# Kernel tuning notes

Measured on AMD Instinct MI355X. Metric: run time of the kernel, lower is better.

The kernel has to match this reference:

```python
import jax, jax.numpy as jnp
import numpy as np

N = 50000      # nodes
E = 800000     # edges (avg degree 16)
D = 128        # in_channels == hidden_channels (required by x*M + x_hat*~M)
OUT = 64       # fc out_channels


def _linear_params(key, out_f, in_f):
    # torch.nn.Linear default init: U(-1/sqrt(in), 1/sqrt(in))
    bound = 1.0 / np.sqrt(in_f)
    kw, kb = jax.random.split(key)
    W = jax.random.uniform(kw, (out_f, in_f), jnp.float32, -bound, bound)
    b = jax.random.uniform(kb, (out_f,), jnp.float32, -bound, bound)
    return W, b


def setup_inputs() -> dict:
    key = jax.random.key(0)
    ks = jax.random.split(key, 8)
    x = jax.random.normal(ks[0], (N, D), jnp.float32)
    edge_index = jax.random.randint(ks[1], (2, E), 0, N, dtype=jnp.int64)
    edge_weight = jax.random.uniform(ks[2], (E,), jnp.float32)
    M = jax.random.randint(ks[3], (N, D), 0, 2) > 0  # bool mask
    W1, b1 = _linear_params(ks[4], D, D)
    W2, b2 = _linear_params(ks[5], D, D)
    W3, b3 = _linear_params(ks[6], D, D)
    Wf, bf = _linear_params(ks[7], OUT, D)
    # extra Parameter `bias` in each FPLayer is zero-initialized
    z = jnp.zeros((D,), jnp.float32)
    return {"edge_index": edge_index, "edge_weight": edge_weight, "x": x, "M": M,
            "W1": W1, "b1": b1, "bias1": z, "W2": W2, "b2": b2, "bias2": z,
            "W3": W3, "b3": b3, "bias3": z, "Wf": Wf, "bf": bf}


def reference(edge_index, edge_weight, x, M,
              W1, b1, bias1, W2, b2, bias2, W3, b3, bias3, Wf, bf):
    row, col = edge_index[0], edge_index[1]
    n = x.shape[0]
    # symmetric degree normalization based on destination-node in-degree
    deg = jax.ops.segment_sum(jnp.ones(row.shape[0], x.dtype), col, num_segments=n)
    safe = jnp.where(deg > 0, deg, 1.0)
    dinv = jnp.where(deg > 0, 1.0 / jnp.sqrt(safe), 0.0)
    norm = dinv[row] * dinv[col]  # [E]  (edge_weight is unused by message())

    def fp_layer(x_tilde, W, b, bias):
        msg = norm[:, None] * x_tilde[row]                      # [E, D] gather
        agg = jax.ops.segment_sum(msg, col, num_segments=n)     # [N, D] scatter-add
        return agg @ W.T + b + bias

    # conv1: x_hat = 0 -> x_tilde = x*M
    h = jax.nn.relu(fp_layer(jnp.where(M, x, 0.0), W1, b1, bias1))
    h = jax.nn.relu(fp_layer(jnp.where(M, x, h), W2, b2, bias2))
    h = jax.nn.relu(fp_layer(jnp.where(M, x, h), W3, b3, bias3))
    return h @ Wf.T + bf
```

## Files before the change

### kernel.cpp

```cpp
#include <hip/hip_runtime.h>

#define DD 128
#define OUTF 64
#define SCAP 64
#define NBUCK 8
#define PB_CAP 224
#define CHB 96
#define SCATB (NBUCK * CHB)

typedef __attribute__((ext_vector_type(8))) _Float16 fp16x8;
typedef __attribute__((ext_vector_type(8))) unsigned short ushort8;
typedef __attribute__((ext_vector_type(4))) float floatx4;

union h16 { _Float16 f; unsigned short u; };

__global__ __launch_bounds__(256) void setup_kernel(
    const int* __restrict__ ei, unsigned long long* __restrict__ pairbuf,
    int* __restrict__ pcnt, int* __restrict__ cursor,
    int E, int n,
    const float* __restrict__ W1, const float* __restrict__ W2,
    const float* __restrict__ W3, const float* __restrict__ Wf,
    _Float16* __restrict__ Bh1, _Float16* __restrict__ Bl1,
    _Float16* __restrict__ Bh2, _Float16* __restrict__ Bl2,
    _Float16* __restrict__ Bh3, _Float16* __restrict__ Bl3,
    _Float16* __restrict__ Bhf, _Float16* __restrict__ Blf,
    int nbA) {
    int bid = blockIdx.x;
    int t = threadIdx.x;
    if (bid < nbA) {
        __shared__ int lcnt[NBUCK];
        __shared__ int s_any;
        for (int z = bid * 256 + t; z < n; z += nbA * 256) cursor[z] = 0;
        if (t < NBUCK) lcnt[t] = 0;
        if (t == 0) s_any = 0;
        __syncthreads();
        int e0 = bid * 1024;
        int es = min(e0 + t * 4, E - 1);
        if (ei[2 * es + 1] != 0) s_any = 1;
        __syncthreads();
        bool is64 = (s_any == 0);
        float binv = (float)NBUCK / (float)n;
        for (int j = 0; j < 4; j++) {
            int e = e0 + j * 256 + t;
            if (e < E) {
                int r, c;
                if (is64) {
                    const long long* p = (const long long*)ei;
                    r = (int)p[e];
                    c = (int)p[(size_t)E + e];
                } else {
                    r = ei[e];
                    c = ei[E + e];
                }
                r = min(max(r, 0), n - 1);
                c = min(max(c, 0), n - 1);
                int b = min(NBUCK - 1, (int)((float)c * binv));
                int pos = atomicAdd(&lcnt[b], 1);
                if (pos < PB_CAP)
                    pairbuf[((size_t)bid * NBUCK + b) * PB_CAP + pos] =
                        ((unsigned long long)(unsigned)c << 32) | (unsigned)r;
            }
        }
        __syncthreads();
        if (t < NBUCK) pcnt[bid * NBUCK + t] = min(lcnt[t], PB_CAP);
    } else {
        int tid = (bid - nbA) * 256 + t;
        const float* W; _Float16 *Bh, *Bl; int NT, lt;
        if      (tid < 2048) { W = W1; Bh = Bh1; Bl = Bl1; NT = 8; lt = tid; }
        else if (tid < 4096) { W = W2; Bh = Bh2; Bl = Bl2; NT = 8; lt = tid - 2048; }
        else if (tid < 6144) { W = W3; Bh = Bh3; Bl = Bl3; NT = 8; lt = tid - 4096; }
        else if (tid < 7168) { W = Wf; Bh = Bhf; Bl = Blf; NT = 4; lt = tid - 6144; }
        else return;
        int lane = lt & 63;
        int g = lt >> 6;
        int nt = g % NT;
        int chunk = g / NT;
        int o = nt * 16 + (lane & 15);
        int k = chunk * 32 + (lane >> 4) * 8;
        const float* src = W + o * 128 + k;
#pragma unroll
        for (int j = 0; j < 8; j++) {
            float a = src[j];
            _Float16 h = (_Float16)a;
            Bh[(size_t)lt * 8 + j] = h;
            Bl[(size_t)lt * 8 + j] = (_Float16)(a - (float)h);
        }
    }
}

__global__ __launch_bounds__(256) void scatter_kernel(
    const unsigned long long* __restrict__ pairbuf,
    const int* __restrict__ pcnt,
    int* __restrict__ cursor, int* __restrict__ slot, int nbA) {
    int b = blockIdx.x & (NBUCK - 1);
    int chunk = blockIdx.x >> 3;
    int t = threadIdx.x;
    for (int i = chunk; i < nbA; i += CHB) {
        int cnt = pcnt[i * NBUCK + b];
        const unsigned long long* pp = pairbuf + ((size_t)i * NBUCK + b) * PB_CAP;
        for (int j = t; j < cnt; j += 256) {
            unsigned long long pr = pp[j];
            int c = (int)(pr >> 32);
            int r = (int)(unsigned)pr;
            int pos = atomicAdd(&cursor[c], 1);
            if (pos < SCAP)
                slot[(size_t)c * SCAP + pos] = r;
        }
    }
}

__global__ __launch_bounds__(256) void scale_kernel(
    const int* __restrict__ cursor,
    const float* __restrict__ x, const void* __restrict__ Mv,
    _Float16* __restrict__ xs0, float* __restrict__ dinv, int ndTot) {
    int t = threadIdx.x;
    size_t idx = (size_t)blockIdx.x * 2048 + (size_t)t * 8;
    bool act = (idx + 8 <= (size_t)ndTot);
    __shared__ int s_u8;
    if (t == 0) s_u8 = 0;
    __syncthreads();
    size_t ps = idx + 1;
    if (ps >= (size_t)ndTot) ps = (size_t)ndTot - 1;
    if (((const unsigned char*)Mv)[ps] != 0) s_u8 = 1;
    __syncthreads();
    if (!act) return;
    float4 xa = *(const float4*)&x[idx];
    float4 xb = *(const float4*)&x[idx + 4];
    int m[8];
    if (s_u8) {
        const unsigned char* mp = (const unsigned char*)Mv + idx;
#pragma unroll
        for (int j = 0; j < 8; j++) m[j] = mp[j];
    } else {
        const int* mp = (const int*)Mv + idx;
#pragma unroll
        for (int j = 0; j < 8; j++) m[j] = mp[j];
    }
    int node = (int)(idx >> 7);
    int deg = cursor[node];
    float dv = deg > 0 ? rsqrtf((float)deg) : 0.0f;
    if ((idx & 127) == 0) dinv[node] = dv;
    float xf[8] = {xa.x, xa.y, xa.z, xa.w, xb.x, xb.y, xb.z, xb.w};
    ushort8 o;
#pragma unroll
    for (int j = 0; j < 8; j++) {
        h16 h;
        h.f = (_Float16)(dv * xf[j]);
        o[j] = m[j] ? h.u : (unsigned short)0xFFFF;
    }
    *(ushort8*)&xs0[idx] = o;
}

template <int SENT>
__global__ __launch_bounds__(256) void agg_kernel(const _Float16* __restrict__ xin,
                                                  const int* __restrict__ cursor,
                                                  const int* __restrict__ slot,
                                                  const float* __restrict__ dinv,
                                                  _Float16* __restrict__ A, int n) {
    int wave = (blockIdx.x * 256 + threadIdx.x) >> 6;
    if (wave >= n) return;
    int lane = threadIdx.x & 63;
    int sid = lane >> 4;
    int li = lane & 15;
    int cnt = min(cursor[wave], SCAP);
    float dc = dinv[wave];
    const int* sl = slot + (size_t)wave * SCAP;
    float acc[8] = {0.f, 0.f, 0.f, 0.f, 0.f, 0.f, 0.f, 0.f};
    for (int k = 0; k < cnt; k += 16) {
        int i0 = k + sid;
        int i1 = k + 4 + sid;
        int i2 = k + 8 + sid;
        int i3 = k + 12 + sid;
        int r0 = sl[min(i0, cnt - 1)];
        int r1 = sl[min(i1, cnt - 1)];
        int r2 = sl[min(i2, cnt - 1)];
        int r3 = sl[min(i3, cnt - 1)];
        float m0 = i0 < cnt ? 1.0f : 0.0f;
        float m1 = i1 < cnt ? 1.0f : 0.0f;
        float m2 = i2 < cnt ? 1.0f : 0.0f;
        float m3 = i3 < cnt ? 1.0f : 0.0f;
        if (SENT) {
            ushort8 u0 = *(const ushort8*)&xin[(size_t)r0 * DD + li * 8];
            ushort8 u1 = *(const ushort8*)&xin[(size_t)r1 * DD + li * 8];
            ushort8 u2 = *(const ushort8*)&xin[(size_t)r2 * DD + li * 8];
            ushort8 u3 = *(const ushort8*)&xin[(size_t)r3 * DD + li * 8];
#pragma unroll
            for (int j = 0; j < 8; j++) {
                h16 t0, t1, t2, t3;
                t0.u = (u0[j] == (unsigned short)0xFFFF) ? (unsigned short)0 : u0[j];
                t1.u = (u1[j] == (unsigned short)0xFFFF) ? (unsigned short)0 : u1[j];
                t2.u = (u2[j] == (unsigned short)0xFFFF) ? (unsigned short)0 : u2[j];
                t3.u = (u3[j] == (unsigned short)0xFFFF) ? (unsigned short)0 : u3[j];
                acc[j] += m0 * (float)t0.f + m1 * (float)t1.f
                        + m2 * (float)t2.f + m3 * (float)t3.f;
            }
        } else {
            fp16x8 v0 = *(const fp16x8*)&xin[(size_t)r0 * DD + li * 8];
            fp16x8 v1 = *(const fp16x8*)&xin[(size_t)r1 * DD + li * 8];
            fp16x8 v2 = *(const fp16x8*)&xin[(size_t)r2 * DD + li * 8];
            fp16x8 v3 = *(const fp16x8*)&xin[(size_t)r3 * DD + li * 8];
#pragma unroll
            for (int j = 0; j < 8; j++) {
                acc[j] += m0 * (float)v0[j] + m1 * (float)v1[j]
                        + m2 * (float)v2[j] + m3 * (float)v3[j];
            }
        }
    }
#pragma unroll
    for (int j = 0; j < 8; j++) {
        acc[j] += __shfl_xor(acc[j], 16);
        acc[j] += __shfl_xor(acc[j], 32);
    }
    if (sid == 0) {
        fp16x8 o;
#pragma unroll
        for (int j = 0; j < 8; j++) o[j] = (_Float16)(dc * acc[j]);
        *(fp16x8*)&A[(size_t)wave * DD + li * 8] = o;
    }
}

template <int MODE>
__global__ __launch_bounds__(256) void gemm_mfma(const _Float16* __restrict__ A,
                                                 const _Float16* __restrict__ Bh,
                                                 const _Float16* __restrict__ Bl,
                                                 const float* __restrict__ b,
                                                 const float* __restrict__ bias,
                                                 const float* __restrict__ dinv,
                                                 const _Float16* __restrict__ B2h,
                                                 const _Float16* __restrict__ B2l,
                                                 const float* __restrict__ b2,
                                                 float* __restrict__ out_f,
                                                 const _Float16* __restrict__ xs0,
                                                 _Float16* __restrict__ xt_out,
                                                 int n) {
    __shared__ __align__(16) _Float16 sh[4][16][136];
    int wid = (blockIdx.x * 256 + threadIdx.x) >> 6;
    int nwaves = n >> 4;
    if (wid >= nwaves) return;
    int n0 = wid * 16;
    int lane = threadIdx.x & 63;
    int li = lane & 15;
    int quad = lane >> 4;
    int wv = (threadIdx.x >> 6) & 3;

    floatx4 acc[8];
#pragma unroll
    for (int nt = 0; nt < 8; nt++)
        acc[nt] = (floatx4){0.f, 0.f, 0.f, 0.f};

    const _Float16* arow = A + (size_t)(n0 + li) * DD + quad * 8;
#pragma unroll
    for (int chunk = 0; chunk < 4; chunk++) {
        fp16x8 a = *(const fp16x8*)(arow + chunk * 32);
#pragma unroll
        for (int nt = 0; nt < 8; nt++) {
            size_t boff = (size_t)(((chunk * 8 + nt) << 6) + lane) * 8;
            fp16x8 b_h = *(const fp16x8*)&Bh[boff];
            fp16x8 b_l = *(const fp16x8*)&Bl[boff];
            acc[nt] = __builtin_amdgcn_mfma_f32_16x16x32_f16(a, b_h, acc[nt], 0, 0, 0);
            acc[nt] = __builtin_amdgcn_mfma_f32_16x16x32_f16(a, b_l, acc[nt], 0, 0, 0);
        }
    }

    float dvr[4] = {1.f, 1.f, 1.f, 1.f};
    if (MODE == 0) {
        float4 dv4 = *(const float4*)&dinv[n0 + quad * 4];
        dvr[0] = dv4.x; dvr[1] = dv4.y; dvr[2] = dv4.z; dvr[3] = dv4.w;
    }
#pragma unroll
    for (int nt = 0; nt < 8; nt++) {
        int o = nt * 16 + li;
        float bb = b[o] + bias[o];
#pragma unroll
        for (int reg = 0; reg < 4; reg++) {
            float v = fmaxf(acc[nt][reg] + bb, 0.0f);
            if (MODE == 0) v *= dvr[reg];
            sh[wv][quad * 4 + reg][o] = (_Float16)v;
        }
    }
    __asm__ volatile("s_waitcnt lgkmcnt(0)" ::: "memory");

    if (MODE == 0) {
#pragma unroll
        for (int it = 0; it < 4; it++) {
            int node = it * 4 + quad;
            size_t ix = (size_t)(n0 + node) * DD + li * 8;
            fp16x8 hv = *(const fp16x8*)&sh[wv][node][li * 8];
            fp16x8 xv = *(const fp16x8*)&xs0[ix];
            ushort8 xb = *(const ushort8*)&xs0[ix];
            fp16x8 o;
#pragma unroll
            for (int j = 0; j < 8; j++)
                o[j] = (xb[j] == (unsigned short)0xFFFF) ? hv[j] : xv[j];
            *(fp16x8*)&xt_out[ix] = o;
        }
    } else {
        floatx4 acc2[4];
#pragma unroll
        for (int nt = 0; nt < 4; nt++)
            acc2[nt] = (floatx4){0.f, 0.f, 0.f, 0.f};
#pragma unroll
        for (int chunk = 0; chunk < 4; chunk++) {
            fp16x8 a2 = *(const fp16x8*)&sh[wv][li][chunk * 32 + quad * 8];
#pragma unroll
            for (int nt = 0; nt < 4; nt++) {
                size_t boff = (size_t)(((chunk * 4 + nt) << 6) + lane) * 8;
                fp16x8 b_h = *(const fp16x8*)&B2h[boff];
                fp16x8 b_l = *(const fp16x8*)&B2l[boff];
                acc2[nt] = __builtin_amdgcn_mfma_f32_16x16x32_f16(a2, b_h, acc2[nt], 0, 0, 0);
                acc2[nt] = __builtin_amdgcn_mfma_f32_16x16x32_f16(a2, b_l, acc2[nt], 0, 0, 0);
            }
        }
        __asm__ volatile("s_waitcnt lgkmcnt(0)" ::: "memory");
        float* shf = (float*)&sh[wv][0][0];
#pragma unroll
        for (int nt = 0; nt < 4; nt++) {
            int o = nt * 16 + li;
            float bb = b2[o];
#pragma unroll
            for (int reg = 0; reg < 4; reg++)
                shf[(quad * 4 + reg) * 68 + o] = acc2[nt][reg] + bb;
        }
        __asm__ volatile("s_waitcnt lgkmcnt(0)" ::: "memory");
#pragma unroll
        for (int it = 0; it < 4; it++) {
            int node = it * 4 + quad;
            float4 v = *(const float4*)&shf[node * 68 + li * 4];
            *(float4*)&out_f[(size_t)(n0 + node) * OUTF + li * 4] = v;
        }
    }
}

extern "C" void kernel_launch(void* const* d_in, const int* in_sizes, int n_in,
                              void* d_out, int out_size, void* d_ws, size_t ws_size,
                              hipStream_t stream) {
    const int*   ei    = (const int*)d_in[0];
    const float* x     = (const float*)d_in[2];
    const void*  M     = d_in[3];
    const float* W1    = (const float*)d_in[4];
    const float* b1    = (const float*)d_in[5];
    const float* bias1 = (const float*)d_in[6];
    const float* W2    = (const float*)d_in[7];
    const float* b2    = (const float*)d_in[8];
    const float* bias2 = (const float*)d_in[9];
    const float* W3    = (const float*)d_in[10];
    const float* b3    = (const float*)d_in[11];
    const float* bias3 = (const float*)d_in[12];
    const float* Wf    = (const float*)d_in[13];
    const float* bf    = (const float*)d_in[14];

    const int E = in_sizes[1];
    const int N = in_sizes[2] / DD;
    const int ND = N * DD;

    char* w = (char*)d_ws;
    size_t off = 0;
    auto alloc = [&](size_t bytes) -> char* {
        char* p = w + off;
        off = (off + bytes + 255) & ~(size_t)255;
        return p;
    };
    const int nbA = (E + 1023) / 1024;
    int*   cursor = (int*)  alloc((size_t)N * 4);
    int*   slot   = (int*)  alloc((size_t)N * SCAP * 4);
    float* dinv   = (float*)alloc((size_t)N * 4);
    unsigned long long* pairbuf =
        (unsigned long long*)alloc((size_t)nbA * NBUCK * PB_CAP * 8);
    int*   pcnt   = (int*)  alloc((size_t)nbA * NBUCK * 4);
    _Float16* xs0  = (_Float16*)alloc((size_t)ND * 2);
    _Float16* xt   = (_Float16*)alloc((size_t)ND * 2);
    _Float16* Aa   = (_Float16*)alloc((size_t)ND * 2);
    _Float16* Bh1 = (_Float16*)alloc(128 * 128 * 2);
    _Float16* Bl1 = (_Float16*)alloc(128 * 128 * 2);
    _Float16* Bh2 = (_Float16*)alloc(128 * 128 * 2);
    _Float16* Bl2 = (_Float16*)alloc(128 * 128 * 2);
    _Float16* Bh3 = (_Float16*)alloc(128 * 128 * 2);
    _Float16* Bl3 = (_Float16*)alloc(128 * 128 * 2);
    _Float16* Bhf = (_Float16*)alloc(64 * 128 * 2);
    _Float16* Blf = (_Float16*)alloc(64 * 128 * 2);
    (void)ws_size;

    const int nbPk = 28;
    const int nScale = (ND + 2047) / 2048;

    setup_kernel<<<nbA + nbPk, 256, 0, stream>>>(
        ei, pairbuf, pcnt, cursor, E, N,
        W1, W2, W3, Wf,
        Bh1, Bl1, Bh2, Bl2, Bh3, Bl3, Bhf, Blf,
        nbA);
    scatter_kernel<<<SCATB, 256, 0, stream>>>(pairbuf, pcnt, cursor, slot, nbA);
    scale_kernel<<<nScale, 256, 0, stream>>>(cursor, x, M, xs0, dinv, ND);

    int nwaves = N / 16;
    int gGrid = (nwaves * 64 + 255) / 256;
    int aggGrid = (N * 64 + 255) / 256;

    agg_kernel<1><<<aggGrid, 256, 0, stream>>>(xs0, cursor, slot, dinv, Aa, N);
    gemm_mfma<0><<<gGrid, 256, 0, stream>>>(Aa, Bh1, Bl1, b1, bias1, dinv,
                                            nullptr, nullptr, nullptr, nullptr,
                                            xs0, xt, N);
    agg_kernel<0><<<aggGrid, 256, 0, stream>>>(xt, cursor, slot, dinv, Aa, N);
    gemm_mfma<0><<<gGrid, 256, 0, stream>>>(Aa, Bh2, Bl2, b2, bias2, dinv,
                                            nullptr, nullptr, nullptr, nullptr,
                                            xs0, xt, N);
    agg_kernel<0><<<aggGrid, 256, 0, stream>>>(xt, cursor, slot, dinv, Aa, N);
    gemm_mfma<1><<<gGrid, 256, 0, stream>>>(Aa, Bh3, Bl3, b3, bias3, nullptr,
                                            Bhf, Blf, bf, (float*)d_out,
                                            nullptr, nullptr, N);
}
```

Baseline: 298.3 us.

## Restructure aggregation into column-quarter passes with per-node lane groups

```diff
diff --git a/kernel.cpp b/kernel.cpp
--- a/kernel.cpp
+++ b/kernel.cpp
@@ -112,7 +112,8 @@
 __global__ __launch_bounds__(256) void scale_kernel(
     const int* __restrict__ cursor,
     const float* __restrict__ x, const void* __restrict__ Mv,
-    _Float16* __restrict__ xs0, float* __restrict__ dinv, int ndTot) {
+    _Float16* __restrict__ xs0, _Float16* __restrict__ xz0,
+    float* __restrict__ dinv, int ndTot) {
     int t = threadIdx.x;
     size_t idx = (size_t)blockIdx.x * 2048 + (size_t)t * 8;
     bool act = (idx + 8 <= (size_t)ndTot);
@@ -141,82 +142,63 @@
     float dv = deg > 0 ? rsqrtf((float)deg) : 0.0f;
     if ((idx & 127) == 0) dinv[node] = dv;
     float xf[8] = {xa.x, xa.y, xa.z, xa.w, xb.x, xb.y, xb.z, xb.w};
-    ushort8 o;
+    ushort8 os, oz;
 #pragma unroll
     for (int j = 0; j < 8; j++) {
         h16 h;
         h.f = (_Float16)(dv * xf[j]);
-        o[j] = m[j] ? h.u : (unsigned short)0xFFFF;
-    }
-    *(ushort8*)&xs0[idx] = o;
-}
-
-template <int SENT>
+        os[j] = m[j] ? h.u : (unsigned short)0xFFFF;
+        oz[j] = m[j] ? h.u : (unsigned short)0;
+    }
+    *(ushort8*)&xs0[idx] = os;
+    *(ushort8*)&xz0[idx] = oz;
+}
+
 __global__ __launch_bounds__(256) void agg_kernel(const _Float16* __restrict__ xin,
                                                   const int* __restrict__ cursor,
                                                   const int* __restrict__ slot,
                                                   const float* __restrict__ dinv,
-                                                  _Float16* __restrict__ A, int n) {
-    int wave = (blockIdx.x * 256 + threadIdx.x) >> 6;
-    if (wave >= n) return;
+                                                  _Float16* __restrict__ A,
+                                                  int n, int nbq) {
+    int q = blockIdx.x / nbq;
+    int bq = blockIdx.x - q * nbq;
+    int wq = bq * 4 + ((threadIdx.x) >> 6);
+    int nwq = n >> 4;
+    if (wq >= nwq) return;
     int lane = threadIdx.x & 63;
-    int sid = lane >> 4;
-    int li = lane & 15;
-    int cnt = min(cursor[wave], SCAP);
-    float dc = dinv[wave];
-    const int* sl = slot + (size_t)wave * SCAP;
+    int ng = lane >> 2;
+    int dl = lane & 3;
+    int node = wq * 16 + ng;
+    int cnt = min(cursor[node], SCAP);
+    float dc = dinv[node];
+    const int* sl = slot + (size_t)node * SCAP;
+    const _Float16* xq = xin + q * 32 + dl * 8;
     float acc[8] = {0.f, 0.f, 0.f, 0.f, 0.f, 0.f, 0.f, 0.f};
-    for (int k = 0; k < cnt; k += 16) {
-        int i0 = k + sid;
-        int i1 = k + 4 + sid;
-        int i2 = k + 8 + sid;
-        int i3 = k + 12 + sid;
-        int r0 = sl[min(i0, cnt - 1)];
-        int r1 = sl[min(i1, cnt - 1)];
-        int r2 = sl[min(i2, cnt - 1)];
-        int r3 = sl[min(i3, cnt - 1)];
-        float m0 = i0 < cnt ? 1.0f : 0.0f;
-        float m1 = i1 < cnt ? 1.0f : 0.0f;
-        float m2 = i2 < cnt ? 1.0f : 0.0f;
-        float m3 = i3 < cnt ? 1.0f : 0.0f;
-        if (SENT) {
-            ushort8 u0 = *(const ushort8*)&xin[(size_t)r0 * DD + li * 8];
-            ushort8 u1 = *(const ushort8*)&xin[(size_t)r1 * DD + li * 8];
-            ushort8 u2 = *(const ushort8*)&xin[(size_t)r2 * DD + li * 8];
-            ushort8 u3 = *(const ushort8*)&xin[(size_t)r3 * DD + li * 8];
-#pragma unroll
-            for (int j = 0; j < 8; j++) {
-                h16 t0, t1, t2, t3;
-                t0.u = (u0[j] == (unsigned short)0xFFFF) ? (unsigned short)0 : u0[j];
-                t1.u = (u1[j] == (unsigned short)0xFFFF) ? (unsigned short)0 : u1[j];
-                t2.u = (u2[j] == (unsigned short)0xFFFF) ? (unsigned short)0 : u2[j];
-                t3.u = (u3[j] == (unsigned short)0xFFFF) ? (unsigned short)0 : u3[j];
-                acc[j] += m0 * (float)t0.f + m1 * (float)t1.f
-                        + m2 * (float)t2.f + m3 * (float)t3.f;
-            }
-        } else {
-            fp16x8 v0 = *(const fp16x8*)&xin[(size_t)r0 * DD + li * 8];
-            fp16x8 v1 = *(const fp16x8*)&xin[(size_t)r1 * DD + li * 8];
-            fp16x8 v2 = *(const fp16x8*)&xin[(size_t)r2 * DD + li * 8];
-            fp16x8 v3 = *(const fp16x8*)&xin[(size_t)r3 * DD + li * 8];
-#pragma unroll
-            for (int j = 0; j < 8; j++) {
-                acc[j] += m0 * (float)v0[j] + m1 * (float)v1[j]
-                        + m2 * (float)v2[j] + m3 * (float)v3[j];
-            }
-        }
-    }
-#pragma unroll
-    for (int j = 0; j < 8; j++) {
-        acc[j] += __shfl_xor(acc[j], 16);
-        acc[j] += __shfl_xor(acc[j], 32);
-    }
-    if (sid == 0) {
-        fp16x8 o;
-#pragma unroll
-        for (int j = 0; j < 8; j++) o[j] = (_Float16)(dc * acc[j]);
-        *(fp16x8*)&A[(size_t)wave * DD + li * 8] = o;
-    }
+    for (int k = 0; k < cnt; k += 4) {
+        const int4 s4 = *(const int4*)&sl[k];
+        int r0 = min(max(s4.x, 0), n - 1);
+        int r1 = min(max(s4.y, 0), n - 1);
+        int r2 = min(max(s4.z, 0), n - 1);
+        int r3 = min(max(s4.w, 0), n - 1);
+        float m1 = (k + 1 < cnt) ? 1.0f : 0.0f;
+        float m2 = (k + 2 < cnt) ? 1.0f : 0.0f;
+        float m3 = (k + 3 < cnt) ? 1.0f : 0.0f;
+        fp16x8 v0 = *(const fp16x8*)&xq[(size_t)r0 * DD];
+        fp16x8 v1 = *(const fp16x8*)&xq[(size_t)r1 * DD];
+        fp16x8 v2 = *(const fp16x8*)&xq[(size_t)r2 * DD];
+        fp16x8 v3 = *(const fp16x8*)&xq[(size_t)r3 * DD];
+#pragma unroll
+        for (int j = 0; j < 8; j++) {
+            acc[j] += (float)v0[j];
+            acc[j] += m1 * (float)v1[j];
+            acc[j] += m2 * (float)v2[j];
+            acc[j] += m3 * (float)v3[j];
+        }
+    }
+    fp16x8 o;
+#pragma unroll
+    for (int j = 0; j < 8; j++) o[j] = (_Float16)(dc * acc[j]);
+    *(fp16x8*)&A[(size_t)node * DD + q * 32 + dl * 8] = o;
 }
 
 template <int MODE>
@@ -368,6 +350,7 @@
         (unsigned long long*)alloc((size_t)nbA * NBUCK * PB_CAP * 8);
     int*   pcnt   = (int*)  alloc((size_t)nbA * NBUCK * 4);
     _Float16* xs0  = (_Float16*)alloc((size_t)ND * 2);
+    _Float16* xz0  = (_Float16*)alloc((size_t)ND * 2);
     _Float16* xt   = (_Float16*)alloc((size_t)ND * 2);
     _Float16* Aa   = (_Float16*)alloc((size_t)ND * 2);
     _Float16* Bh1 = (_Float16*)alloc(128 * 128 * 2);
@@ -389,21 +372,23 @@
         Bh1, Bl1, Bh2, Bl2, Bh3, Bl3, Bhf, Blf,
         nbA);
     scatter_kernel<<<SCATB, 256, 0, stream>>>(pairbuf, pcnt, cursor, slot, nbA);
-    scale_kernel<<<nScale, 256, 0, stream>>>(cursor, x, M, xs0, dinv, ND);
+    scale_kernel<<<nScale, 256, 0, stream>>>(cursor, x, M, xs0, xz0, dinv, ND);
 
     int nwaves = N / 16;
     int gGrid = (nwaves * 64 + 255) / 256;
-    int aggGrid = (N * 64 + 255) / 256;
-
-    agg_kernel<1><<<aggGrid, 256, 0, stream>>>(xs0, cursor, slot, dinv, Aa, N);
+    const int nwq = N / 16;
+    const int nbq = (nwq + 3) / 4;
+    const int aggGrid = 4 * nbq;
+
+    agg_kernel<<<aggGrid, 256, 0, stream>>>(xz0, cursor, slot, dinv, Aa, N, nbq);
     gemm_mfma<0><<<gGrid, 256, 0, stream>>>(Aa, Bh1, Bl1, b1, bias1, dinv,
                                             nullptr, nullptr, nullptr, nullptr,
                                             xs0, xt, N);
-    agg_kernel<0><<<aggGrid, 256, 0, stream>>>(xt, cursor, slot, dinv, Aa, N);
+    agg_kernel<<<aggGrid, 256, 0, stream>>>(xt, cursor, slot, dinv, Aa, N, nbq);
     gemm_mfma<0><<<gGrid, 256, 0, stream>>>(Aa, Bh2, Bl2, b2, bias2, dinv,
                                             nullptr, nullptr, nullptr, nullptr,
                                             xs0, xt, N);
-    agg_kernel<0><<<aggGrid, 256, 0, stream>>>(xt, cursor, slot, dinv, Aa, N);
+    agg_kernel<<<aggGrid, 256, 0, stream>>>(xt, cursor, slot, dinv, Aa, N, nbq);
     gemm_mfma<1><<<gGrid, 256, 0, stream>>>(Aa, Bh3, Bl3, b3, bias3, nullptr,
                                             Bhf, Blf, bf, (float*)d_out,
                                             nullptr, nullptr, N);
```

Result: slower. 360.5 us (+20.8%).

## Pad neighbor slots with zero-row index and process two tiles per GEMM wave

Applied to the files above, without the earlier changes.

```diff
diff --git a/kernel.cpp b/kernel.cpp
--- a/kernel.cpp
+++ b/kernel.cpp
@@ -110,11 +110,18 @@
 }
 
 __global__ __launch_bounds__(256) void scale_kernel(
-    const int* __restrict__ cursor,
+    const int* __restrict__ cursor, int* __restrict__ slot,
     const float* __restrict__ x, const void* __restrict__ Mv,
-    _Float16* __restrict__ xs0, float* __restrict__ dinv, int ndTot) {
+    _Float16* __restrict__ xs0, _Float16* __restrict__ xz0,
+    _Float16* __restrict__ xt, float* __restrict__ dinv,
+    int nNodes, int ndTot) {
     int t = threadIdx.x;
     size_t idx = (size_t)blockIdx.x * 2048 + (size_t)t * 8;
+    if (blockIdx.x == 0 && t < 16) {
+        ushort8 z = {0, 0, 0, 0, 0, 0, 0, 0};
+        *(ushort8*)&xz0[(size_t)nNodes * DD + t * 8] = z;
+        *(ushort8*)&xt[(size_t)nNodes * DD + t * 8] = z;
+    }
     bool act = (idx + 8 <= (size_t)ndTot);
     __shared__ int s_u8;
     if (t == 0) s_u8 = 0;
@@ -139,19 +146,26 @@
     int node = (int)(idx >> 7);
     int deg = cursor[node];
     float dv = deg > 0 ? rsqrtf((float)deg) : 0.0f;
-    if ((idx & 127) == 0) dinv[node] = dv;
+    if ((idx & 127) == 0) {
+        dinv[node] = dv;
+        int cnt = min(deg, SCAP);
+        int cu = (cnt + 15) & ~15;
+        for (int i2 = cnt; i2 < cu; i2++)
+            slot[(size_t)node * SCAP + i2] = nNodes;
+    }
     float xf[8] = {xa.x, xa.y, xa.z, xa.w, xb.x, xb.y, xb.z, xb.w};
-    ushort8 o;
+    ushort8 os, oz;
 #pragma unroll
     for (int j = 0; j < 8; j++) {
         h16 h;
         h.f = (_Float16)(dv * xf[j]);
-        o[j] = m[j] ? h.u : (unsigned short)0xFFFF;
-    }
-    *(ushort8*)&xs0[idx] = o;
-}
-
-template <int SENT>
+        os[j] = m[j] ? h.u : (unsigned short)0xFFFF;
+        oz[j] = m[j] ? h.u : (unsigned short)0;
+    }
+    *(ushort8*)&xs0[idx] = os;
+    *(ushort8*)&xz0[idx] = oz;
+}
+
 __global__ __launch_bounds__(256) void agg_kernel(const _Float16* __restrict__ xin,
                                                   const int* __restrict__ cursor,
                                                   const int* __restrict__ slot,
@@ -163,47 +177,25 @@
     int sid = lane >> 4;
     int li = lane & 15;
     int cnt = min(cursor[wave], SCAP);
+    int cntUp = (cnt + 15) & ~15;
     float dc = dinv[wave];
     const int* sl = slot + (size_t)wave * SCAP;
     float acc[8] = {0.f, 0.f, 0.f, 0.f, 0.f, 0.f, 0.f, 0.f};
-    for (int k = 0; k < cnt; k += 16) {
-        int i0 = k + sid;
-        int i1 = k + 4 + sid;
-        int i2 = k + 8 + sid;
-        int i3 = k + 12 + sid;
-        int r0 = sl[min(i0, cnt - 1)];
-        int r1 = sl[min(i1, cnt - 1)];
-        int r2 = sl[min(i2, cnt - 1)];
-        int r3 = sl[min(i3, cnt - 1)];
-        float m0 = i0 < cnt ? 1.0f : 0.0f;
-        float m1 = i1 < cnt ? 1.0f : 0.0f;
-        float m2 = i2 < cnt ? 1.0f : 0.0f;
-        float m3 = i3 < cnt ? 1.0f : 0.0f;
-        if (SENT) {
-            ushort8 u0 = *(const ushort8*)&xin[(size_t)r0 * DD + li * 8];
-            ushort8 u1 = *(const ushort8*)&xin[(size_t)r1 * DD + li * 8];
-            ushort8 u2 = *(const ushort8*)&xin[(size_t)r2 * DD + li * 8];
-            ushort8 u3 = *(const ushort8*)&xin[(size_t)r3 * DD + li * 8];
-#pragma unroll
-            for (int j = 0; j < 8; j++) {
-                h16 t0, t1, t2, t3;
-                t0.u = (u0[j] == (unsigned short)0xFFFF) ? (unsigned short)0 : u0[j];
-                t1.u = (u1[j] == (unsigned short)0xFFFF) ? (unsigned short)0 : u1[j];
-                t2.u = (u2[j] == (unsigned short)0xFFFF) ? (unsigned short)0 : u2[j];
-                t3.u = (u3[j] == (unsigned short)0xFFFF) ? (unsigned short)0 : u3[j];
-                acc[j] += m0 * (float)t0.f + m1 * (float)t1.f
-                        + m2 * (float)t2.f + m3 * (float)t3.f;
-            }
-        } else {
-            fp16x8 v0 = *(const fp16x8*)&xin[(size_t)r0 * DD + li * 8];
-            fp16x8 v1 = *(const fp16x8*)&xin[(size_t)r1 * DD + li * 8];
-            fp16x8 v2 = *(const fp16x8*)&xin[(size_t)r2 * DD + li * 8];
-            fp16x8 v3 = *(const fp16x8*)&xin[(size_t)r3 * DD + li * 8];
-#pragma unroll
-            for (int j = 0; j < 8; j++) {
-                acc[j] += m0 * (float)v0[j] + m1 * (float)v1[j]
-                        + m2 * (float)v2[j] + m3 * (float)v3[j];
-            }
+    for (int k = 0; k < cntUp; k += 16) {
+        int r0 = sl[k + sid];
+        int r1 = sl[k + 4 + sid];
+        int r2 = sl[k + 8 + sid];
+        int r3 = sl[k + 12 + sid];
+        fp16x8 v0 = *(const fp16x8*)&xin[(size_t)r0 * DD + li * 8];
+        fp16x8 v1 = *(const fp16x8*)&xin[(size_t)r1 * DD + li * 8];
+        fp16x8 v2 = *(const fp16x8*)&xin[(size_t)r2 * DD + li * 8];
+        fp16x8 v3 = *(const fp16x8*)&xin[(size_t)r3 * DD + li * 8];
+#pragma unroll
+        for (int j = 0; j < 8; j++) {
+            acc[j] += (float)v0[j];
+            acc[j] += (float)v1[j];
+            acc[j] += (float)v2[j];
+            acc[j] += (float)v3[j];
         }
     }
 #pragma unroll
@@ -234,101 +226,117 @@
                                                  _Float16* __restrict__ xt_out,
                                                  int n) {
     __shared__ __align__(16) _Float16 sh[4][16][136];
-    int wid = (blockIdx.x * 256 + threadIdx.x) >> 6;
+    int pid = (blockIdx.x * 256 + threadIdx.x) >> 6;
     int nwaves = n >> 4;
-    if (wid >= nwaves) return;
-    int n0 = wid * 16;
+    int npairs = (nwaves + 1) >> 1;
+    if (pid >= npairs) return;
+    int t0 = pid * 2;
+    int t1 = t0 + 1;
+    bool has1 = (t1 < nwaves);
     int lane = threadIdx.x & 63;
     int li = lane & 15;
     int quad = lane >> 4;
     int wv = (threadIdx.x >> 6) & 3;
 
-    floatx4 acc[8];
-#pragma unroll
-    for (int nt = 0; nt < 8; nt++)
-        acc[nt] = (floatx4){0.f, 0.f, 0.f, 0.f};
-
-    const _Float16* arow = A + (size_t)(n0 + li) * DD + quad * 8;
+    floatx4 acc0[8], acc1[8];
+#pragma unroll
+    for (int nt = 0; nt < 8; nt++) {
+        acc0[nt] = (floatx4){0.f, 0.f, 0.f, 0.f};
+        acc1[nt] = (floatx4){0.f, 0.f, 0.f, 0.f};
+    }
+
+    const _Float16* arow0 = A + (size_t)(t0 * 16 + li) * DD + quad * 8;
+    int t1s = has1 ? t1 : t0;
+    const _Float16* arow1 = A + (size_t)(t1s * 16 + li) * DD + quad * 8;
 #pragma unroll
     for (int chunk = 0; chunk < 4; chunk++) {
-        fp16x8 a = *(const fp16x8*)(arow + chunk * 32);
+        fp16x8 a0 = *(const fp16x8*)(arow0 + chunk * 32);
+        fp16x8 a1 = *(const fp16x8*)(arow1 + chunk * 32);
 #pragma unroll
         for (int nt = 0; nt < 8; nt++) {
             size_t boff = (size_t)(((chunk * 8 + nt) << 6) + lane) * 8;
             fp16x8 b_h = *(const fp16x8*)&Bh[boff];
             fp16x8 b_l = *(const fp16x8*)&Bl[boff];
-            acc[nt] = __builtin_amdgcn_mfma_f32_16x16x32_f16(a, b_h, acc[nt], 0, 0, 0);
-            acc[nt] = __builtin_amdgcn_mfma_f32_16x16x32_f16(a, b_l, acc[nt], 0, 0, 0);
-        }
-    }
-
-    float dvr[4] = {1.f, 1.f, 1.f, 1.f};
-    if (MODE == 0) {
-        float4 dv4 = *(const float4*)&dinv[n0 + quad * 4];
-        dvr[0] = dv4.x; dvr[1] = dv4.y; dvr[2] = dv4.z; dvr[3] = dv4.w;
-    }
-#pragma unroll
-    for (int nt = 0; nt < 8; nt++) {
-        int o = nt * 16 + li;
-        float bb = b[o] + bias[o];
-#pragma unroll
-        for (int reg = 0; reg < 4; reg++) {
-            float v = fmaxf(acc[nt][reg] + bb, 0.0f);
-            if (MODE == 0) v *= dvr[reg];
-            sh[wv][quad * 4 + reg][o] = (_Float16)v;
-        }
-    }
-    __asm__ volatile("s_waitcnt lgkmcnt(0)" ::: "memory");
-
-    if (MODE == 0) {
-#pragma unroll
-        for (int it = 0; it < 4; it++) {
-            int node = it * 4 + quad;
-            size_t ix = (size_t)(n0 + node) * DD + li * 8;
-            fp16x8 hv = *(const fp16x8*)&sh[wv][node][li * 8];
-            fp16x8 xv = *(const fp16x8*)&xs0[ix];
-            ushort8 xb = *(const ushort8*)&xs0[ix];
-            fp16x8 o;
-#pragma unroll
-            for (int j = 0; j < 8; j++)
-                o[j] = (xb[j] == (unsigned short)0xFFFF) ? hv[j] : xv[j];
-            *(fp16x8*)&xt_out[ix] = o;
-        }
-    } else {
-        floatx4 acc2[4];
-#pragma unroll
-        for (int nt = 0; nt < 4; nt++)
-            acc2[nt] = (floatx4){0.f, 0.f, 0.f, 0.f};
-#pragma unroll
-        for (int chunk = 0; chunk < 4; chunk++) {
-            fp16x8 a2 = *(const fp16x8*)&sh[wv][li][chunk * 32 + quad * 8];
+            acc0[nt] = __builtin_amdgcn_mfma_f32_16x16x32_f16(a0, b_h, acc0[nt], 0, 0, 0);
+            acc0[nt] = __builtin_amdgcn_mfma_f32_16x16x32_f16(a0, b_l, acc0[nt], 0, 0, 0);
+            acc1[nt] = __builtin_amdgcn_mfma_f32_16x16x32_f16(a1, b_h, acc1[nt], 0, 0, 0);
+            acc1[nt] = __builtin_amdgcn_mfma_f32_16x16x32_f16(a1, b_l, acc1[nt], 0, 0, 0);
+        }
+    }
+
+    auto epilogue = [&](const floatx4 (&acc)[8], int tb) {
+        int n0 = tb * 16;
+        __asm__ volatile("s_waitcnt lgkmcnt(0)" ::: "memory");
+        float dvr[4] = {1.f, 1.f, 1.f, 1.f};
+        if (MODE == 0) {
+            float4 dv4 = *(const float4*)&dinv[n0 + quad * 4];
+            dvr[0] = dv4.x; dvr[1] = dv4.y; dvr[2] = dv4.z; dvr[3] = dv4.w;
+        }
+#pragma unroll
+        for (int nt = 0; nt < 8; nt++) {
+            int o = nt * 16 + li;
+            float bb = b[o] + bias[o];
+#pragma unroll
+            for (int reg = 0; reg < 4; reg++) {
+                float v = fmaxf(acc[nt][reg] + bb, 0.0f);
+                if (MODE == 0) v *= dvr[reg];
+                sh[wv][quad * 4 + reg][o] = (_Float16)v;
+            }
+        }
+        __asm__ volatile("s_waitcnt lgkmcnt(0)" ::: "memory");
+
+        if (MODE == 0) {
+#pragma unroll
+            for (int it = 0; it < 4; it++) {
+                int node = it * 4 + quad;
+                size_t ix = (size_t)(n0 + node) * DD + li * 8;
+                fp16x8 hv = *(const fp16x8*)&sh[wv][node][li * 8];
+                fp16x8 xv = *(const fp16x8*)&xs0[ix];
+                ushort8 xb = *(const ushort8*)&xs0[ix];
+                fp16x8 o;
+#pragma unroll
+                for (int j = 0; j < 8; j++)
+                    o[j] = (xb[j] == (unsigned short)0xFFFF) ? hv[j] : xv[j];
+                *(fp16x8*)&xt_out[ix] = o;
+            }
+        } else {
+            floatx4 acc2[4];
+#pragma unroll
+            for (int nt = 0; nt < 4; nt++)
+                acc2[nt] = (floatx4){0.f, 0.f, 0.f, 0.f};
+#pragma unroll
+            for (int chunk = 0; chunk < 4; chunk++) {
+                fp16x8 a2 = *(const fp16x8*)&sh[wv][li][chunk * 32 + quad * 8];
+#pragma unroll
+                for (int nt = 0; nt < 4; nt++) {
+                    size_t boff = (size_t)(((chunk * 4 + nt) << 6) + lane) * 8;
+                    fp16x8 b_h = *(const fp16x8*)&B2h[boff];
+                    fp16x8 b_l = *(const fp16x8*)&B2l[boff];
+                    acc2[nt] = __builtin_amdgcn_mfma_f32_16x16x32_f16(a2, b_h, acc2[nt], 0, 0, 0);
+                    acc2[nt] = __builtin_amdgcn_mfma_f32_16x16x32_f16(a2, b_l, acc2[nt], 0, 0, 0);
+                }
+            }
+            __asm__ volatile("s_waitcnt lgkmcnt(0)" ::: "memory");
+            float* shf = (float*)&sh[wv][0][0];
 #pragma unroll
             for (int nt = 0; nt < 4; nt++) {
-                size_t boff = (size_t)(((chunk * 4 + nt) << 6) + lane) * 8;
-                fp16x8 b_h = *(const fp16x8*)&B2h[boff];
-                fp16x8 b_l = *(const fp16x8*)&B2l[boff];
-                acc2[nt] = __builtin_amdgcn_mfma_f32_16x16x32_f16(a2, b_h, acc2[nt], 0, 0, 0);
-                acc2[nt] = __builtin_amdgcn_mfma_f32_16x16x32_f16(a2, b_l, acc2[nt], 0, 0, 0);
-            }
-        }
-        __asm__ volatile("s_waitcnt lgkmcnt(0)" ::: "memory");
-        float* shf = (float*)&sh[wv][0][0];
-#pragma unroll
-        for (int nt = 0; nt < 4; nt++) {
-            int o = nt * 16 + li;
-            float bb = b2[o];
-#pragma unroll
-            for (int reg = 0; reg < 4; reg++)
-                shf[(quad * 4 + reg) * 68 + o] = acc2[nt][reg] + bb;
-        }
-        __asm__ volatile("s_waitcnt lgkmcnt(0)" ::: "memory");
-#pragma unroll
-        for (int it = 0; it < 4; it++) {
-            int node = it * 4 + quad;
-            float4 v = *(const float4*)&shf[node * 68 + li * 4];
-            *(float4*)&out_f[(size_t)(n0 + node) * OUTF + li * 4] = v;
-        }
-    }
+                int o = nt * 16 + li;
+                float bb = b2[o];
+#pragma unroll
+                for (int reg = 0; reg < 4; reg++)
+                    shf[(quad * 4 + reg) * 68 + o] = acc2[nt][reg] + bb;
+            }
+            __asm__ volatile("s_waitcnt lgkmcnt(0)" ::: "memory");
+#pragma unroll
+            for (int it = 0; it < 4; it++) {
+                int node = it * 4 + quad;
+                float4 v = *(const float4*)&shf[node * 68 + li * 4];
+                *(float4*)&out_f[(size_t)(n0 + node) * OUTF + li * 4] = v;
+            }
+        }
+    };
+    epilogue(acc0, t0);
+    if (has1) epilogue(acc1, t1);
 }
 
 extern "C" void kernel_launch(void* const* d_in, const int* in_sizes, int n_in,
@@ -368,7 +376,8 @@
         (unsigned long long*)alloc((size_t)nbA * NBUCK * PB_CAP * 8);
     int*   pcnt   = (int*)  alloc((size_t)nbA * NBUCK * 4);
     _Float16* xs0  = (_Float16*)alloc((size_t)ND * 2);
-    _Float16* xt   = (_Float16*)alloc((size_t)ND * 2);
+    _Float16* xz0  = (_Float16*)alloc(((size_t)ND + DD) * 2);
+    _Float16* xt   = (_Float16*)alloc(((size_t)ND + DD) * 2);
     _Float16* Aa   = (_Float16*)alloc((size_t)ND * 2);
     _Float16* Bh1 = (_Float16*)alloc(128 * 128 * 2);
     _Float16* Bl1 = (_Float16*)alloc(128 * 128 * 2);
@@ -389,21 +398,23 @@
         Bh1, Bl1, Bh2, Bl2, Bh3, Bl3, Bhf, Blf,
         nbA);
     scatter_kernel<<<SCATB, 256, 0, stream>>>(pairbuf, pcnt, cursor, slot, nbA);
-    scale_kernel<<<nScale, 256, 0, stream>>>(cursor, x, M, xs0, dinv, ND);
+    scale_kernel<<<nScale, 256, 0, stream>>>(cursor, slot, x, M, xs0, xz0, xt,
+                                             dinv, N, ND);
 
     int nwaves = N / 16;
-    int gGrid = (nwaves * 64 + 255) / 256;
+    int npairs = (nwaves + 1) / 2;
+    int gGrid = (npairs * 64 + 255) / 256;
     int aggGrid = (N * 64 + 255) / 256;
 
-    agg_kernel<1><<<aggGrid, 256, 0, stream>>>(xs0, cursor, slot, dinv, Aa, N);
+    agg_kernel<<<aggGrid, 256, 0, stream>>>(xz0, cursor, slot, dinv, Aa, N);
     gemm_mfma<0><<<gGrid, 256, 0, stream>>>(Aa, Bh1, Bl1, b1, bias1, dinv,
                                             nullptr, nullptr, nullptr, nullptr,
                                             xs0, xt, N);
-    agg_kernel<0><<<aggGrid, 256, 0, stream>>>(xt, cursor, slot, dinv, Aa, N);
+    agg_kernel<<<aggGrid, 256, 0, stream>>>(xt, cursor, slot, dinv, Aa, N);
     gemm_mfma<0><<<gGrid, 256, 0, stream>>>(Aa, Bh2, Bl2, b2, bias2, dinv,
                                             nullptr, nullptr, nullptr, nullptr,
                                             xs0, xt, N);
-    agg_kernel<0><<<aggGrid, 256, 0, stream>>>(xt, cursor, slot, dinv, Aa, N);
+    agg_kernel<<<aggGrid, 256, 0, stream>>>(xt, cursor, slot, dinv, Aa, N);
     gemm_mfma<1><<<gGrid, 256, 0, stream>>>(Aa, Bh3, Bl3, b3, bias3, nullptr,
                                             Bhf, Blf, bf, (float*)d_out,
                                             nullptr, nullptr, N);
```

After: 300.9 us. No clear change (+0.9%).
